# Kernel optimization log

Measured on AMD Instinct MI355X. Metric: run time of the kernel, lower is better.

## Reference

```python
import jax, jax.numpy as jnp
import numpy as np
from jax import lax

A_NUM = 3
STRIDES = (4, 8, 16, 32, 64)
LEVEL_HW = ((128, 208), (64, 104), (32, 52), (16, 26), (8, 13))
IMG_H, IMG_W = 512.0, 832.0
PRE_NMS, POST_NMS, NMS_TH = 6000, 1000, 0.7


def _base_anchors(base_size, ratios=(0.5, 1.0, 2.0), scales=(8.0,)):
    ratios = np.asarray(ratios, np.float64)
    scales = np.asarray(scales, np.float64)
    cx = cy = (base_size - 1) / 2.0
    size = float(base_size) * float(base_size)
    ws = np.round(np.sqrt(size / ratios))
    hs = np.round(ws * ratios)
    ws = (ws[:, None] * scales[None, :]).reshape(-1)
    hs = (hs[:, None] * scales[None, :]).reshape(-1)
    return np.stack([cx - 0.5 * (ws - 1), cy - 0.5 * (hs - 1),
                     cx + 0.5 * (ws - 1), cy + 0.5 * (hs - 1)], axis=1)


def _all_anchors():
    # generate_anchors_global: per-level shifted grids, concatenated, order (h, w, a)
    out = []
    for stride, (h, w) in zip(STRIDES, LEVEL_HW):
        base = _base_anchors(stride)  # [A,4]
        sx = np.arange(w) * stride
        sy = np.arange(h) * stride
        sx, sy = np.meshgrid(sx, sy)
        shifts = np.stack([sx.ravel(), sy.ravel(), sx.ravel(), sy.ravel()], axis=1)
        anc = (shifts[:, None, :] + base[None, :, :]).reshape(-1, 4)  # [H*W*A,4]
        out.append(anc)
    return np.concatenate(out, axis=0).astype(np.float32)

_ANCHORS = _all_anchors()


def _conv(x, w, b, pad):
    y = lax.conv_general_dilated(x, w, (1, 1), [(pad, pad), (pad, pad)],
                                 dimension_numbers=('NCHW', 'OIHW', 'NCHW'))
    return y + b[None, :, None, None]


def _bbox_transform_inv(anchors, deltas):
    w = anchors[:, 2] - anchors[:, 0] + 1.0
    h = anchors[:, 3] - anchors[:, 1] + 1.0
    cx = anchors[:, 0] + 0.5 * w
    cy = anchors[:, 1] + 0.5 * h
    dx, dy, dw, dh = deltas[:, 0], deltas[:, 1], deltas[:, 2], deltas[:, 3]
    pcx = dx * w + cx
    pcy = dy * h + cy
    pw = jnp.exp(dw) * w
    ph = jnp.exp(dh) * h
    return jnp.stack([pcx - 0.5 * pw, pcy - 0.5 * ph,
                      pcx + 0.5 * pw, pcy + 0.5 * ph], axis=1)


def _iou_one_to_many(box, boxes):
    area = (boxes[:, 2] - boxes[:, 0] + 1.0) * (boxes[:, 3] - boxes[:, 1] + 1.0)
    area_b = (box[2] - box[0] + 1.0) * (box[3] - box[1] + 1.0)
    xx1 = jnp.maximum(box[0], boxes[:, 0])
    yy1 = jnp.maximum(box[1], boxes[:, 1])
    xx2 = jnp.minimum(box[2], boxes[:, 2])
    yy2 = jnp.minimum(box[3], boxes[:, 3])
    iw = jnp.maximum(0.0, xx2 - xx1 + 1.0)
    ih = jnp.maximum(0.0, yy2 - yy1 + 1.0)
    inter = iw * ih
    return inter / (area + area_b - inter)


def _nms_fixed(boxes, scores, thresh, max_out):
    # greedy NMS with a fixed number of iterations (jit-friendly)
    def body(s, _):
        i = jnp.argmax(s)
        valid = s[i] > -jnp.inf
        ious = _iou_one_to_many(boxes[i], boxes)
        s2 = jnp.where(ious > thresh, -jnp.inf, s)
        s2 = s2.at[i].set(-jnp.inf)
        return s2, (i, valid)
    _, (idx, valid) = lax.scan(body, scores, None, length=max_out)
    return idx, valid


def _rpn_forward(feats, im_info, rpn_conv_w, rpn_conv_b, rpn_score_w,
                 rpn_score_b, rpn_bbox_w, rpn_bbox_b):
    fg_scores, bbox_deltas = [], []
    for p in feats:
        H, W = p.shape[-2], p.shape[-1]
        f = _conv(p, rpn_conv_w, rpn_conv_b, 1)              # [1,512,H,W]
        cls = _conv(f, rpn_score_w, rpn_score_b, 0)          # [1,2A,H,W]
        # _reshape_layer(.,2) + softmax(dim=1) + _reshape_layer back + permute
        prob = jax.nn.softmax(cls.reshape(1, 2, A_NUM, H, W), axis=1)
        prob = prob.reshape(1, 2 * A_NUM, H, W).transpose(0, 2, 3, 1)  # [1,H,W,2A]
        fg = prob[..., A_NUM:].reshape(-1)                    # fg prob, order (h,w,a)
        bb = _conv(f, rpn_bbox_w, rpn_bbox_b, 0).transpose(0, 2, 3, 1).reshape(-1, 4)
        fg_scores.append(fg)
        bbox_deltas.append(bb)
    scores = jnp.concatenate(fg_scores, axis=0)              # [Ntot]
    deltas = jnp.concatenate(bbox_deltas, axis=0)            # [Ntot,4]
    anchors = jnp.asarray(_ANCHORS)

    proposals = _bbox_transform_inv(anchors, deltas)
    # clip to image
    proposals = jnp.stack([
        jnp.clip(proposals[:, 0], 0.0, im_info[1] - 1.0),
        jnp.clip(proposals[:, 1], 0.0, im_info[0] - 1.0),
        jnp.clip(proposals[:, 2], 0.0, im_info[1] - 1.0),
        jnp.clip(proposals[:, 3], 0.0, im_info[0] - 1.0)], axis=1)

    # pre-NMS top-k by score
    top_scores, order = lax.top_k(scores, PRE_NMS)
    top_boxes = proposals[order]
    keep, valid = _nms_fixed(top_boxes, top_scores, NMS_TH, POST_NMS)
    vmask = valid.astype(top_boxes.dtype)[:, None]
    sel_boxes = top_boxes[keep] * vmask
    sel_scores = top_scores[keep][:, None] * vmask
    rois = jnp.concatenate([jnp.zeros((POST_NMS, 1), sel_boxes.dtype), sel_boxes], axis=1)
    return jnp.concatenate([rois, sel_scores], axis=1)        # [POST_NMS, 6]


def setup_inputs() -> dict:
    key = jax.random.key(0)
    ks = jax.random.split(key, 12)
    chans = 256
    feats = {}
    for i, (name, (h, w)) in enumerate(zip(['p2', 'p3', 'p4', 'p5', 'p6'], LEVEL_HW)):
        feats[name] = jax.random.normal(ks[i], (1, chans, h, w), jnp.float32)
    inp = dict(feats)
    inp['im_info'] = jnp.array([IMG_H, IMG_W, 1.0], jnp.float32)
    inp['rpn_conv_w'] = jax.random.normal(ks[5], (512, chans, 3, 3), jnp.float32) * 0.03
    inp['rpn_conv_b'] = jnp.zeros((512,), jnp.float32)
    inp['rpn_score_w'] = jax.random.normal(ks[6], (2 * A_NUM, 512, 1, 1), jnp.float32) * 0.03
    inp['rpn_score_b'] = jnp.zeros((2 * A_NUM,), jnp.float32)
    inp['rpn_bbox_w'] = jax.random.normal(ks[7], (4 * A_NUM, 512, 1, 1), jnp.float32) * 0.01
    inp['rpn_bbox_b'] = jnp.zeros((4 * A_NUM,), jnp.float32)
    return inp


def reference(p2, p3, p4, p5, p6, im_info, rpn_conv_w, rpn_conv_b,
              rpn_score_w, rpn_score_b, rpn_bbox_w, rpn_bbox_b):
    return _rpn_forward([p2, p3, p4, p5, p6], im_info, rpn_conv_w, rpn_conv_b,
                        rpn_score_w, rpn_score_b, rpn_bbox_w, rpn_bbox_b)
```

## Files before the change

kernel.cpp:

```cpp
#include <hip/hip_runtime.h>
#include <stdint.h>

#define N_ANCH   106392
#define PRE_NMS  6000
#define POST_NMS 1000
#define POOL_CAP 8192
#define NMS_BLKS 94
#define SUP_W    96

static __device__ const int    LV_H[5]      = {128, 64, 32, 16, 8};
static __device__ const int    LV_W[5]      = {208, 104, 52, 26, 13};
static __device__ const int    LV_STRIDE[5] = {4, 8, 16, 32, 64};
static __device__ const int    LV_PIX[5]    = {26624, 6656, 1664, 416, 104};
static __device__ const int    LV_TILE0[6]  = {0, 416, 520, 546, 553, 555};
static __device__ const int    LV_AOFF[6]   = {0, 79872, 99840, 104832, 106080, 106392};
static __device__ const int    GPOFF[6]     = {0, 26624, 33280, 34944, 35360, 35464};
static __device__ const double BASE_ANCH[5][3][4] = {
  {{-22.,-10.,25.,13.},   {-14.,-14.,17.,17.},    {-10.,-22.,13.,25.}},
  {{-40.,-20.,47.,27.},   {-28.,-28.,35.,35.},    {-20.,-44.,27.,51.}},
  {{-84.,-40.,99.,55.},   {-56.,-56.,71.,71.},    {-36.,-80.,51.,95.}},
  {{-164.,-72.,195.,103.},{-112.,-112.,143.,143.},{-76.,-168.,107.,199.}},
  {{-332.,-152.,395.,215.},{-224.,-224.,287.,287.},{-148.,-328.,211.,391.}}
};

__device__ __forceinline__ uint32_t sort32f(float f) {
  uint32_t u = __float_as_uint(f);
  return ((int)u < 0) ? ~u : (u | 0x80000000u);
}
__device__ __forceinline__ uint64_t sort64(double d) {
  uint64_t u = (uint64_t)__double_as_longlong(d);
  return ((long long)u < 0) ? ~u : (u | 0x8000000000000000ull);
}

__device__ __forceinline__ double combf(const float* sw, const float* bw, int c, int j) {
  if (j < 3) return (double)sw[(3 + j) * 512 + c] - (double)sw[j * 512 + c];
  return (double)bw[(j - 3) * 512 + c];
}

__global__ __launch_bounds__(256) void k_weff_part(const float* __restrict__ cw,
                                                   const float* __restrict__ sw,
                                                   const float* __restrict__ bw,
                                                   double* __restrict__ Wpart) {
  int chunk = blockIdx.x / 9;
  int tb = blockIdx.x % 9;
  int t = tb * 256 + threadIdx.x;
  int c0 = chunk * 32;
  double acc[15];
#pragma unroll
  for (int j = 0; j < 15; ++j) acc[j] = 0.0;
#pragma unroll 1
  for (int c = c0; c < c0 + 32; ++c) {
    double v = (double)cw[c * 2304 + t];
#pragma unroll
    for (int j = 0; j < 15; ++j) acc[j] += v * combf(sw, bw, c, j);
  }
  double* o = Wpart + (((size_t)chunk * 2304 + t) << 4);
#pragma unroll
  for (int j = 0; j < 15; ++j) o[j] = acc[j];
  o[15] = 0.0;
}

__global__ __launch_bounds__(256) void k_weff_fin(const double* __restrict__ Wpart,
                                                  const float* __restrict__ cb,
                                                  const float* __restrict__ sb,
                                                  const float* __restrict__ bb,
                                                  const float* __restrict__ sw,
                                                  const float* __restrict__ bw,
                                                  double* __restrict__ Weff,
                                                  double* __restrict__ fb,
                                                  float4* __restrict__ w3,
                                                  float* __restrict__ fb32) {
  if (blockIdx.x == 9) {
    __shared__ double ps[15][16];
    int tid = threadIdx.x;
    if (tid < 240) {
      int j = tid >> 4, part = tid & 15;
      double s = 0.0;
      for (int c = part * 32; c < part * 32 + 32; ++c)
        s += (double)cb[c] * combf(sw, bw, c, j);
      ps[j][part] = s;
    }
    __syncthreads();
    if (tid < 15) {
      double s = 0.0;
#pragma unroll
      for (int part = 0; part < 16; ++part) s += ps[tid][part];
      s += (tid < 3) ? ((double)sb[3 + tid] - (double)sb[tid]) : (double)bb[tid - 3];
      fb[tid] = s;
      if (tid < 3) fb32[tid] = (float)s;
    }
    if (tid == 15) fb32[3] = 0.f;
    return;
  }
  int t = blockIdx.x * 256 + threadIdx.x;
  double acc[15];
#pragma unroll
  for (int j = 0; j < 15; ++j) acc[j] = 0.0;
#pragma unroll 1
  for (int chunk = 0; chunk < 16; ++chunk) {
    const double* p = Wpart + (((size_t)chunk * 2304 + t) << 4);
#pragma unroll
    for (int j = 0; j < 15; ++j) acc[j] += p[j];
  }
  double* o = Weff + ((size_t)t << 4);
#pragma unroll
  for (int j = 0; j < 15; ++j) o[j] = acc[j];
  o[15] = 0.0;
  float4 wf;
  wf.x = (float)acc[0]; wf.y = (float)acc[1]; wf.z = (float)acc[2]; wf.w = 0.f;
  w3[t] = wf;
}

__global__ __launch_bounds__(256) void k_w5(const double* __restrict__ Weff,
                                            double* __restrict__ w5) {
  int idx = blockIdx.x * 256 + threadIdx.x;
  if (idx >= 2304 * 3) return;
  int t = idx / 3, a = idx % 3;
  int ci = t / 9, t9 = t % 9;
  const double* src = Weff + ((size_t)t << 4);
  double* dst = w5 + (size_t)ci * 192 + (size_t)(t9 * 3 + a) * 6;
  int jd = 3 + 4 * a;
  dst[0] = src[jd + 0];
  dst[1] = src[jd + 1];
  dst[2] = src[jd + 2];
  dst[3] = src[jd + 3];
  dst[4] = src[a];
  dst[5] = 0.0;
}

__device__ __forceinline__ void load9(float v[9], const float* __restrict__ ib,
                                      const bool rok[3], const bool cok[3],
                                      const int roff[3]) {
#pragma unroll
  for (int ky = 0; ky < 3; ++ky)
#pragma unroll
    for (int kx = 0; kx < 3; ++kx)
      v[ky * 3 + kx] = (rok[ky] && cok[kx]) ? ib[roff[ky] + kx] : 0.0f;
}

__global__ __launch_bounds__(256) void k_fast(
    const float* __restrict__ p0, const float* __restrict__ p1,
    const float* __restrict__ p2, const float* __restrict__ p3,
    const float* __restrict__ p4,
    const float4* __restrict__ w3, float* __restrict__ qpart) {
  __shared__ float4 w3s[1152];
  __shared__ float red[4][64][3];
  int tid = threadIdx.x, wv = tid >> 6, ln = tid & 63;
  int t = blockIdx.x >> 1, hf = blockIdx.x & 1;
  int cbase = hf * 128;
  for (int i = tid; i < 1152; i += 256) w3s[i] = w3[cbase * 9 + i];
  int L = 0;
  while (L < 4 && t >= LV_TILE0[L + 1]) ++L;
  const float* inL = (L == 0) ? p0 : (L == 1) ? p1 : (L == 2) ? p2 : (L == 3) ? p3 : p4;
  int H = LV_H[L], W = LV_W[L], HW = H * W, PIX = LV_PIX[L];
  int pix = (t - LV_TILE0[L]) * 64 + ln;
  if (pix >= PIX) pix = PIX - 1;
  int h = pix / W, w = pix % W;
  bool rok[3], cok[3];
  int roff[3];
#pragma unroll
  for (int ky = 0; ky < 3; ++ky) {
    int iy = h + ky - 1;
    rok[ky] = (iy >= 0 && iy < H);
    roff[ky] = iy * W + w - 1;
  }
#pragma unroll
  for (int kx = 0; kx < 3; ++kx) {
    int ix = w + kx - 1;
    cok[kx] = (ix >= 0 && ix < W);
  }
  int lci0 = wv * 32;
  const float* ibn = inL + (size_t)(cbase + lci0) * HW;
  float vn[9];
  load9(vn, ibn, rok, cok, roff);
  __syncthreads();
  float a0 = 0.f, a1 = 0.f, a2 = 0.f;
#pragma unroll 1
  for (int c = 0; c < 32; ++c) {
    float vc[9];
#pragma unroll
    for (int q = 0; q < 9; ++q) vc[q] = vn[q];
    if (c < 31) {
      ibn += HW;
      load9(vn, ibn, rok, cok, roff);
    }
    const float4* wr = w3s + (lci0 + c) * 9;
#pragma unroll
    for (int t9 = 0; t9 < 9; ++t9) {
      float4 wt = wr[t9];
      float vv = vc[t9];
      a0 += vv * wt.x; a1 += vv * wt.y; a2 += vv * wt.z;
    }
  }
  red[wv][ln][0] = a0; red[wv][ln][1] = a1; red[wv][ln][2] = a2;
  __syncthreads();
  if (wv == 0) {
    float* o = qpart + ((size_t)(t * 2 + hf) * 64 + ln) * 3;
#pragma unroll
    for (int a = 0; a < 3; ++a)
      o[a] = (red[0][ln][a] + red[1][ln][a]) + (red[2][ln][a] + red[3][ln][a]);
  }
}

__global__ __launch_bounds__(256) void k_fcomb(
    const float* __restrict__ qpart, const float* __restrict__ fb32,
    float* __restrict__ logits32, uint32_t* __restrict__ hist) {
  int tid = threadIdx.x, ln = tid & 63;
  int t = blockIdx.x * 4 + (tid >> 6);
  if (t >= 555) return;
  int L = 0;
  while (L < 4 && t >= LV_TILE0[L + 1]) ++L;
  int PIX = LV_PIX[L];
  int pix = (t - LV_TILE0[L]) * 64 + ln;
  if (pix >= PIX) return;
  const float* q0 = qpart + ((size_t)(t * 2 + 0) * 64 + ln) * 3;
  const float* q1 = qpart + ((size_t)(t * 2 + 1) * 64 + ln) * 3;
  int gbase = LV_AOFF[L] + pix * 3;
#pragma unroll
  for (int a = 0; a < 3; ++a) {
    float f = (q0[a] + q1[a]) + fb32[a];
    logits32[gbase + a] = f;
    atomicAdd(&hist[sort32f(f) >> 16], 1u);
  }
}

__global__ __launch_bounds__(1024) void k_edge(const uint32_t* __restrict__ hist,
                                               uint32_t* __restrict__ cnts) {
  __shared__ uint32_t cs[1024];
  __shared__ uint32_t g_grp, g_suf;
  int t = threadIdx.x, wv = t >> 6, ln = t & 63;
#pragma unroll 4
  for (int r = 0; r < 64; ++r) {
    int g = r * 16 + wv;
    uint32_t x = hist[g * 64 + ln];
#pragma unroll
    for (int off = 32; off > 0; off >>= 1) x += __shfl_down(x, off);
    if (ln == 0) cs[g] = x;
  }
  __syncthreads();
  for (int off = 1; off < 1024; off <<= 1) {
    uint32_t v = cs[t] + ((t + off < 1024) ? cs[t + off] : 0u);
    __syncthreads();
    cs[t] = v;
    __syncthreads();
  }
  uint32_t sufnext = (t < 1023) ? cs[t + 1] : 0u;
  if (cs[t] >= PRE_NMS && sufnext < PRE_NMS) {
    g_grp = (uint32_t)t;
    g_suf = sufnext;
  }
  __syncthreads();
  if (t < 64) {
    uint32_t grp = g_grp, suf = g_suf;
    uint32_t x = hist[grp * 64 + t];
    uint32_t S = x;
#pragma unroll
    for (int off = 1; off < 64; off <<= 1) {
      uint32_t y = __shfl_down(S, off);
      if (t + off < 64) S += y;
    }
    unsigned long long mask = __ballot(suf + S >= PRE_NMS);
    int hi = 63 - (int)__clzll(mask);
    if (t == hi) {
      uint32_t e = grp * 64 + (uint32_t)hi;
      cnts[1] = (e > 2) ? e - 2 : 0;
    }
  }
}

__global__ __launch_bounds__(256) void k_cnt(const float* __restrict__ logits32,
                                             const uint32_t* __restrict__ cnts,
                                             uint32_t* __restrict__ bcnt) {
  __shared__ uint32_t wc[4];
  int tid = threadIdx.x;
  int i = blockIdx.x * 256 + tid;
  uint32_t edge = cnts[1];
  bool pass = (i < N_ANCH) && ((sort32f(logits32[i]) >> 16) >= edge);
  unsigned long long m = __ballot(pass);
  if ((tid & 63) == 0) wc[tid >> 6] = (uint32_t)__popcll(m);
  __syncthreads();
  if (tid == 0) bcnt[blockIdx.x] = wc[0] + wc[1] + wc[2] + wc[3];
}

__global__ __launch_bounds__(256) void k_fill(const float* __restrict__ logits32,
                                              uint32_t* __restrict__ cnts,
                                              const uint32_t* __restrict__ bcnt,
                                              uint32_t* __restrict__ alist) {
  __shared__ uint32_t red[256];
  __shared__ uint32_t woff[4];
  int tid = threadIdx.x, wv = tid >> 6, ln = tid & 63;
  uint32_t s = 0;
  for (int k = tid; k < blockIdx.x; k += 256) s += bcnt[k];
  red[tid] = s;
  __syncthreads();
#pragma unroll
  for (int off = 128; off > 0; off >>= 1) {
    if (tid < off) red[tid] += red[tid + off];
    __syncthreads();
  }
  uint32_t base = red[0];
  int i = blockIdx.x * 256 + tid;
  uint32_t edge = cnts[1];
  bool pass = (i < N_ANCH) && ((sort32f(logits32[i]) >> 16) >= edge);
  unsigned long long m = __ballot(pass);
  if (ln == 0) woff[wv] = (uint32_t)__popcll(m);
  __syncthreads();
  uint32_t off_in_blk = 0;
  for (int k = 0; k < wv; ++k) off_in_blk += woff[k];
  if (pass) {
    uint32_t pos = base + off_in_blk + (uint32_t)__popcll(m & ((1ull << ln) - 1ull));
    if (pos < POOL_CAP) alist[pos] = (uint32_t)i;
  }
  if (blockIdx.x == ((N_ANCH + 255) / 256 - 1) && tid == 0)
    cnts[0] = base + woff[0] + woff[1] + woff[2] + woff[3];
}

__global__ __launch_bounds__(128) void k_refine(
    const float* __restrict__ p0, const float* __restrict__ p1,
    const float* __restrict__ p2, const float* __restrict__ p3,
    const float* __restrict__ p4,
    const double* __restrict__ w5,
    const uint32_t* __restrict__ alist, const uint32_t* __restrict__ cnts,
    double* __restrict__ ppart) {
  __shared__ int4 wlds[2][768];
  int tid = threadIdx.x, wv = tid >> 6, ln = tid & 63;
  int cnt = (int)cnts[0];
  if (cnt > POOL_CAP) cnt = POOL_CAP;
  int grp = blockIdx.x >> 1, half = blockIdx.x & 1;
  int base = grp * 64;
  if (base >= cnt) return;
  int slot = base + ln;
  if (slot >= cnt) slot = cnt - 1;
  int gi = (int)alist[slot];
  int gpix = gi / 3, a = gi - gpix * 3;
  int L = 0;
  while (L < 4 && gpix >= GPOFF[L + 1]) ++L;
  int pix = gpix - GPOFF[L];
  const float* inL = (L == 0) ? p0 : (L == 1) ? p1 : (L == 2) ? p2 : (L == 3) ? p3 : p4;
  int H = LV_H[L], W = LV_W[L], HW = H * W;
  int h = pix / W, w = pix % W;
  bool rok[3], cok[3];
  int roff[3];
#pragma unroll
  for (int ky = 0; ky < 3; ++ky) {
    int iy = h + ky - 1;
    rok[ky] = (iy >= 0 && iy < H);
    roff[ky] = iy * W + w - 1;
  }
#pragma unroll
  for (int kx = 0; kx < 3; ++kx) {
    int ix = w + kx - 1;
    cok[kx] = (ix >= 0 && ix < W);
  }
  int chunk = half * 2 + wv;
  int ci0 = chunk * 64;
  const char* wbc = (const char*)&wlds[wv][0];
  {
    const int4* gs = (const int4*)((const char*)w5 + (size_t)ci0 * 1536);
    int4 r[12];
#pragma unroll
    for (int i = 0; i < 12; ++i) r[i] = gs[i * 64 + ln];
#pragma unroll
    for (int i = 0; i < 12; ++i) wlds[wv][i * 64 + ln] = r[i];
  }
  double sc = 0.0, d0 = 0.0, d1 = 0.0, d2 = 0.0, d3 = 0.0;
  const float* ibn = inL + (size_t)ci0 * HW;
  float vn[9];
  load9(vn, ibn, rok, cok, roff);
#pragma unroll 1
  for (int k = 0; k < 8; ++k) {
    int4 r[12];
    if (k < 7) {
      const int4* gs =
          (const int4*)((const char*)w5 + (size_t)(ci0 + (k + 1) * 8) * 1536);
#pragma unroll
      for (int i = 0; i < 12; ++i) r[i] = gs[i * 64 + ln];
    }
#pragma unroll 1
    for (int c2 = 0; c2 < 8; ++c2) {
      float vc[9];
#pragma unroll
      for (int q = 0; q < 9; ++q) vc[q] = vn[q];
      int lc = k * 8 + c2;
      if (lc < 63) {
        ibn += HW;
        load9(vn, ibn, rok, cok, roff);
      }
      const char* b2 = wbc + c2 * 1536 + a * 48;
#pragma unroll
      for (int t9 = 0; t9 < 9; ++t9) {
        double vd = (double)vc[t9];
        double2 w01 = *(const double2*)(b2 + t9 * 144);
        double2 w23 = *(const double2*)(b2 + t9 * 144 + 16);
        double  w4  = *(const double*)(b2 + t9 * 144 + 32);
        d0 += vd * w01.x; d1 += vd * w01.y;
        d2 += vd * w23.x; d3 += vd * w23.y;
        sc += vd * w4;
      }
    }
    if (k < 7) {
#pragma unroll
      for (int i = 0; i < 12; ++i) wlds[wv][i * 64 + ln] = r[i];
    }
  }
  double* o = ppart + ((size_t)slot * 4 + chunk) * 5;
  o[0] = sc; o[1] = d0; o[2] = d1; o[3] = d2; o[4] = d3;
}

__global__ __launch_bounds__(256) void k_comb(
    const uint32_t* __restrict__ alist, const uint32_t* __restrict__ cnts,
    const double* __restrict__ ppart, const double* __restrict__ fb,
    double* __restrict__ logits, double* __restrict__ deltas,
    uint64_t* __restrict__ pkey) {
  int e = blockIdx.x * 256 + threadIdx.x;
  int cnt = (int)cnts[0];
  if (cnt > POOL_CAP) cnt = POOL_CAP;
  if (blockIdx.x * 256 >= cnt) return;
  if (e >= cnt) return;
  int gi = (int)alist[e];
  int a = gi - (gi / 3) * 3;
  const double* p = ppart + (size_t)e * 20;
  double f[5];
#pragma unroll
  for (int j = 0; j < 5; ++j)
    f[j] = ((p[0 + j] + p[5 + j]) + p[10 + j]) + p[15 + j];
  int js = a, jd = 3 + 4 * a;
  double lg = f[0] + fb[js];
  logits[gi] = lg;
  deltas[gi * 4 + 0] = f[1] + fb[jd + 0];
  deltas[gi * 4 + 1] = f[2] + fb[jd + 1];
  deltas[gi * 4 + 2] = f[3] + fb[jd + 2];
  deltas[gi * 4 + 3] = f[4] + fb[jd + 3];
  pkey[e] = (sort64(lg) & ~0x1FFFFull) | (uint64_t)(0x1FFFFu - (uint32_t)gi);
}

__global__ __launch_bounds__(256) void k_rank_cnt(const uint32_t* __restrict__ cnts,
                                                  const uint64_t* __restrict__ pkey,
                                                  uint32_t* __restrict__ rank32) {
  __shared__ uint64_t lk[512];
  int t = threadIdx.x;
  int cnt = (int)cnts[0];
  if (cnt > POOL_CAP) cnt = POOL_CAP;
  int it = blockIdx.x >> 4, jc = blockIdx.x & 15;
  int e = it * 256 + t;
  int c0 = jc * 512;
  if (it * 256 >= cnt || c0 >= cnt) return;
  int lim = cnt - c0; if (lim > 512) lim = 512;
  for (int i = t; i < 512; i += 256) lk[i] = (i < lim) ? pkey[c0 + i] : 0ull;
  __syncthreads();
  bool active = e < cnt;
  uint64_t mykey = active ? pkey[e] : ~0ull;
  int r = 0;
#pragma unroll 8
  for (int j = 0; j < 512; ++j) r += (lk[j] > mykey) ? 1 : 0;
  if (active && r) atomicAdd(&rank32[e], (uint32_t)r);
}

__global__ __launch_bounds__(256) void k_scatter(const uint32_t* __restrict__ cnts,
                                                 const uint64_t* __restrict__ pkey,
                                                 const uint32_t* __restrict__ rank32,
                                                 const double* __restrict__ logits,
                                                 const double* __restrict__ deltas,
                                                 const float* __restrict__ im_info,
                                                 double* __restrict__ ss,
                                                 double* __restrict__ sbx,
                                                 float4* __restrict__ bxf,
                                                 float* __restrict__ areaf) {
  int t = threadIdx.x;
  int cnt = (int)cnts[0];
  if (cnt > POOL_CAP) cnt = POOL_CAP;
  int e = blockIdx.x * 256 + t;
  if (blockIdx.x * 256 >= cnt) return;
  if (e >= cnt) return;
  int rank = (int)rank32[e];
  if (rank >= PRE_NMS) return;
  uint64_t mykey = pkey[e];
  int gi = 0x1FFFF - (int)(mykey & 0x1FFFFull);
  int L = 0;
  while (L < 4 && gi >= LV_AOFF[L + 1]) ++L;
  int rel = gi - LV_AOFF[L];
  int pix = rel / 3, a = rel % 3;
  int W = LV_W[L];
  int h = pix / W, w = pix % W;
  double imW1 = (double)im_info[1] - 1.0;
  double imH1 = (double)im_info[0] - 1.0;
  double shx = (double)(w * LV_STRIDE[L]), shy = (double)(h * LV_STRIDE[L]);
  double ax1 = BASE_ANCH[L][a][0] + shx, ay1 = BASE_ANCH[L][a][1] + shy;
  double ax2 = BASE_ANCH[L][a][2] + shx, ay2 = BASE_ANCH[L][a][3] + shy;
  double dx = deltas[gi * 4 + 0], dy = deltas[gi * 4 + 1];
  double dw = deltas[gi * 4 + 2], dh = deltas[gi * 4 + 3];
  double wa = ax2 - ax1 + 1.0, ha = ay2 - ay1 + 1.0;
  double cx = ax1 + 0.5 * wa, cy = ay1 + 0.5 * ha;
  double pcx = dx * wa + cx, pcy = dy * ha + cy;
  double pw = exp(dw) * wa, ph = exp(dh) * ha;
  double x1 = fmin(fmax(pcx - 0.5 * pw, 0.0), imW1);
  double y1 = fmin(fmax(pcy - 0.5 * ph, 0.0), imH1);
  double x2 = fmin(fmax(pcx + 0.5 * pw, 0.0), imW1);
  double y2 = fmin(fmax(pcy + 0.5 * ph, 0.0), imH1);
  ss[rank] = 1.0 / (1.0 + exp(-logits[gi]));
  sbx[rank * 4 + 0] = x1; sbx[rank * 4 + 1] = y1;
  sbx[rank * 4 + 2] = x2; sbx[rank * 4 + 3] = y2;
  float4 bf;
  bf.x = (float)x1; bf.y = (float)y1; bf.z = (float)x2; bf.w = (float)y2;
  bxf[rank] = bf;
  areaf[rank] = (float)((x2 - x1 + 1.0) * (y2 - y1 + 1.0));
}

__device__ __forceinline__ bool iou_gt(const double* A, const double* B) {
  double areaA = (A[2] - A[0] + 1.0) * (A[3] - A[1] + 1.0);
  double areaB = (B[2] - B[0] + 1.0) * (B[3] - B[1] + 1.0);
  double xx1 = fmax(A[0], B[0]), yy1 = fmax(A[1], B[1]);
  double xx2 = fmin(A[2], B[2]), yy2 = fmin(A[3], B[3]);
  double iw = fmax(0.0, xx2 - xx1 + 1.0), ih = fmax(0.0, yy2 - yy1 + 1.0);
  double inter = iw * ih;
  return inter > 0.7 * (areaA + areaB - inter);
}

__global__ __launch_bounds__(256) void k_build(const double* __restrict__ sbx,
                                               const float4* __restrict__ bxf,
                                               const float* __restrict__ areaf,
                                               uint64_t* __restrict__ Sup) {
  __shared__ float cbx[256][5];
  __shared__ float rbx[64][5];
  int blk = blockIdx.x;
  int rtile = blk / 24, ctile = blk % 24;
  int t = threadIdx.x, q = t >> 6, ln = t & 63;
  int r = rtile * 64 + ln;
  int w = ctile * 4 + q;
  {
    int c = ctile * 256 + t;
    float4 b;
    float ar;
    if (c < NMS_BLKS * 64) { b = bxf[c]; ar = areaf[c]; }
    else { b.x = b.y = b.z = b.w = 0.f; ar = 0.f; }
    cbx[t][0] = b.x; cbx[t][1] = b.y; cbx[t][2] = b.z; cbx[t][3] = b.w; cbx[t][4] = ar;
    if (t < 64) {
      int rr = rtile * 64 + t;
      float4 rb = bxf[rr];
      rbx[t][0] = rb.x; rbx[t][1] = rb.y; rbx[t][2] = rb.z; rbx[t][3] = rb.w;
      rbx[t][4] = areaf[rr];
    }
  }
  __syncthreads();
  uint64_t bits = 0ull;
  int j0 = w * 64;
  if (w < NMS_BLKS && j0 + 63 > r) {
    float ax1 = rbx[ln][0], ay1 = rbx[ln][1], ax2 = rbx[ln][2], ay2 = rbx[ln][3];
    float aar = rbx[ln][4];
#pragma unroll 4
    for (int jj = 0; jj < 64; ++jj) {
      int j = j0 + jj;
      if (j <= r) continue;
      int cl = q * 64 + jj;
      float iw = fminf(ax2, cbx[cl][2]) - fmaxf(ax1, cbx[cl][0]) + 1.f;
      float ih = fminf(ay2, cbx[cl][3]) - fmaxf(ay1, cbx[cl][1]) + 1.f;
      float inter = fmaxf(iw, 0.f) * fmaxf(ih, 0.f);
      float d = inter - 0.7f * (aar + cbx[cl][4] - inter);
      bool sup;
      if (d > 4.0f) sup = true;
      else if (d < -4.0f) sup = false;
      else sup = iou_gt(sbx + (size_t)r * 4, sbx + (size_t)j * 4);
      if (sup) bits |= 1ull << jj;
    }
  }
  Sup[(size_t)r * SUP_W + w] = bits;
}

__global__ __launch_bounds__(1024) void k_scan(const uint64_t* __restrict__ Sup,
                                               const double* __restrict__ ss,
                                               const double* __restrict__ sbx,
                                               float* __restrict__ out) {
  __shared__ uint16_t keep[POST_NMS];
  __shared__ uint32_t ext_arr[SUP_W][2];
  __shared__ int s_kcnt, s_done;
  __shared__ int s_pend[2][2];
  int t = threadIdx.x, wv = t >> 6, ln = t & 63;
  for (int i = t; i < SUP_W * 2; i += 1024) ext_arr[i >> 1][i & 1] = 0u;
  if (t == 0) { s_kcnt = 0; s_done = 0; }
  if (t < 4) s_pend[t >> 1][t & 1] = 0;
  uint64_t diag = 0ull, nxt = 0ull;
  if (wv == 0) {
    size_t r = (size_t)ln * SUP_W;
    diag = Sup[r + 0];
    nxt  = Sup[r + 1];
  }
  __syncthreads();
  for (int b = 0; b < NMS_BLKS; ++b) {
    if (wv == 0) {
      uint64_t myrow = diag & ~((2ull << ln) - 1ull);
      uint64_t mynxt = nxt;
      if (b + 1 < NMS_BLKS) {
        size_t r = (size_t)((b + 1) * 64 + ln) * SUP_W;
        diag = Sup[r + (b + 1)];
        nxt  = Sup[r + (b + 2)];
      }
      uint64_t ext = ((uint64_t)ext_arr[b][1] << 32) | ext_arr[b][0];
      int base = b * 64;
      if (base + 63 >= PRE_NMS) {
        int v = PRE_NMS - base;
        ext |= ~((1ull << v) - 1ull);
      }
      int K0 = s_kcnt;
      uint64_t avail;
      {
        uint64_t a0 = ~ext;
        uint32_t alo = __builtin_amdgcn_readfirstlane((uint32_t)a0);
        uint32_t ahi = __builtin_amdgcn_readfirstlane((uint32_t)(a0 >> 32));
        avail = ((uint64_t)ahi << 32) | alo;
      }
      uint32_t mr_lo = (uint32_t)myrow, mr_hi = (uint32_t)(myrow >> 32);
      uint32_t mn_lo = (uint32_t)mynxt, mn_hi = (uint32_t)(mynxt >> 32);
      uint64_t kp = 0ull, extn = 0ull;
      int lim = POST_NMS - K0, nk = 0;
      while (avail && nk < lim) {
        int i2 = __ffsll((unsigned long long)avail) - 1;
        uint32_t rlo = (uint32_t)__builtin_amdgcn_readlane((int)mr_lo, i2);
        uint32_t rhi = (uint32_t)__builtin_amdgcn_readlane((int)mr_hi, i2);
        uint32_t qlo = (uint32_t)__builtin_amdgcn_readlane((int)mn_lo, i2);
        uint32_t qhi = (uint32_t)__builtin_amdgcn_readlane((int)mn_hi, i2);
        kp |= 1ull << i2;
        ++nk;
        extn |= ((uint64_t)qhi << 32) | qlo;
        avail &= ~(((uint64_t)rhi << 32) | rlo);
        avail &= ~(1ull << i2);
      }
      if ((kp >> ln) & 1ull) {
        int pos = K0 + __popcll(kp & ((1ull << ln) - 1ull));
        keep[pos] = (uint16_t)(base + ln);
      }
      if (ln == 0) {
        if ((uint32_t)extn)         atomicOr(&ext_arr[b + 1][0], (uint32_t)extn);
        if ((uint32_t)(extn >> 32)) atomicOr(&ext_arr[b + 1][1],
                                             (uint32_t)(extn >> 32));
        s_kcnt = K0 + nk;
        s_pend[(b + 1) & 1][0] = K0;
        s_pend[(b + 1) & 1][1] = K0 + nk;
        if (K0 + nk >= POST_NMS || b + 1 >= NMS_BLKS) s_done = 1;
      }
    } else {
      int lo = s_pend[b & 1][0], hi = s_pend[b & 1][1];
      if (hi > lo) {
        int tt = t - 64;
        int g = tt / 96, w = tt - g * 96;
        if (w >= b + 1) {
          uint64_t v = 0ull;
          for (int q = lo + g; q < hi; q += 10)
            v |= Sup[(size_t)keep[q] * SUP_W + w];
          if (v) {
            if ((uint32_t)v)         atomicOr(&ext_arr[w][0], (uint32_t)v);
            if ((uint32_t)(v >> 32)) atomicOr(&ext_arr[w][1], (uint32_t)(v >> 32));
          }
        }
      }
    }
    __syncthreads();
    if (s_done) break;
  }
  __syncthreads();
  int KF = s_kcnt;
  for (int r = t; r < POST_NMS; r += 1024) {
    float* o = out + r * 6;
    if (r < KF) {
      int p = keep[r];
      o[0] = 0.f;
      o[1] = (float)sbx[p * 4 + 0];
      o[2] = (float)sbx[p * 4 + 1];
      o[3] = (float)sbx[p * 4 + 2];
      o[4] = (float)sbx[p * 4 + 3];
      o[5] = (float)ss[p];
    } else {
#pragma unroll
      for (int c = 0; c < 6; ++c) o[c] = 0.f;
    }
  }
}

extern "C" void kernel_launch(void* const* d_in, const int* in_sizes, int n_in,
                              void* d_out, int out_size, void* d_ws, size_t ws_size,
                              hipStream_t stream) {
  const float* p0 = (const float*)d_in[0];
  const float* p1 = (const float*)d_in[1];
  const float* p2 = (const float*)d_in[2];
  const float* p3 = (const float*)d_in[3];
  const float* p4 = (const float*)d_in[4];
  const float* im_info = (const float*)d_in[5];
  const float* cw = (const float*)d_in[6];
  const float* cb = (const float*)d_in[7];
  const float* sw = (const float*)d_in[8];
  const float* sb = (const float*)d_in[9];
  const float* bw = (const float*)d_in[10];
  const float* bb = (const float*)d_in[11];
  char* ws = (char*)d_ws;
  uint32_t* hist    = (uint32_t*)(ws + 0);
  uint32_t* cnts    = (uint32_t*)(ws + 262144);
  double*   fb      = (double*)  (ws + 262208);
  float*    fb32    = (float*)   (ws + 262336);
  double*   logits  = (double*)  (ws + 262352);
  double*   deltas  = (double*)  (ws + 1113488);
  float*    logits32= (float*)   (ws + 4518032);
  float4*   w3      = (float4*)  (ws + 4943600);
  double*   Weff    = (double*)  (ws + 4980464);
  double*   Wpart   = (double*)  (ws + 5275376);
  uint32_t* alist   = (uint32_t*)(ws + 9993968);
  double*   ssort   = (double*)  (ws + 10026736);
  double*   sbx     = (double*)  (ws + 10074864);
  float4*   bxf     = (float4*)  (ws + 10267376);
  float*    areaf   = (float*)   (ws + 10363632);
  uint64_t* Sup     = (uint64_t*)(ws + 10387696);
  uint64_t* pkey    = (uint64_t*)(ws + 15007984);
  uint32_t* rank32  = (uint32_t*)(ws + 15073520);
  uint32_t* bcnt    = hist;
  double*   W5      = Wpart;
  double*   ppart   = (double*)(ws + 5275376 + 524288);
  float*    qpart   = (float*) (ws + 5275376 + 2097152);
  float* out = (float*)d_out;

  hipMemsetAsync(ws, 0, 262208, stream);
  hipMemsetAsync(rank32, 0, 32768, stream);
  k_weff_part<<<144, 256, 0, stream>>>(cw, sw, bw, Wpart);
  k_weff_fin<<<10, 256, 0, stream>>>(Wpart, cb, sb, bb, sw, bw, Weff, fb, w3, fb32);
  k_w5<<<27, 256, 0, stream>>>(Weff, W5);
  k_fast<<<1110, 256, 0, stream>>>(p0, p1, p2, p3, p4, w3, qpart);
  k_fcomb<<<139, 256, 0, stream>>>(qpart, fb32, logits32, hist);
  k_edge<<<1, 1024, 0, stream>>>(hist, cnts);
  k_cnt<<<416, 256, 0, stream>>>(logits32, cnts, bcnt);
  k_fill<<<416, 256, 0, stream>>>(logits32, cnts, bcnt, alist);
  k_refine<<<256, 128, 0, stream>>>(p0, p1, p2, p3, p4, W5, alist, cnts, ppart);
  k_comb<<<32, 256, 0, stream>>>(alist, cnts, ppart, fb, logits, deltas, pkey);
  k_rank_cnt<<<512, 256, 0, stream>>>(cnts, pkey, rank32);
  k_scatter<<<32, 256, 0, stream>>>(cnts, pkey, rank32, logits, deltas, im_info,
                                    ssort, sbx, bxf, areaf);
  k_build<<<94 * 24, 256, 0, stream>>>(sbx, bxf, areaf, Sup);
  k_scan<<<1, 1024, 0, stream>>>(Sup, ssort, sbx, out);
}
```

Before: 408.0 us.

## Deepen NMS scan pipeline: wave0 propagates two blocks ahead, helpers defer loads

The serial NMS scan now has wave 0 read the suppression words for the next two column blocks and OR both into the external mask, instead of only the next block. Because of this, the helper waves can lag one iteration. They issue up to four global loads of Sup rows per block, then combine and atomically apply them in the following iteration, so load latency overlaps wave 0's serial work. The __syncthreads is replaced by an explicit lgkmcnt wait plus s_barrier, which does not wait on outstanding global (vmcnt) loads. This adds register pressure and subtle correctness risk: the delayed masks must land before block b+2 is read, and the barrier no longer orders global memory.

```diff
diff --git a/kernel.cpp b/kernel.cpp
--- a/kernel.cpp
+++ b/kernel.cpp
@@ -578,21 +578,25 @@
   for (int i = t; i < SUP_W * 2; i += 1024) ext_arr[i >> 1][i & 1] = 0u;
   if (t == 0) { s_kcnt = 0; s_done = 0; }
   if (t < 4) s_pend[t >> 1][t & 1] = 0;
-  uint64_t diag = 0ull, nxt = 0ull;
+  uint64_t diag = 0ull, nxt1 = 0ull, nxt2 = 0ull;
   if (wv == 0) {
     size_t r = (size_t)ln * SUP_W;
     diag = Sup[r + 0];
-    nxt  = Sup[r + 1];
-  }
+    nxt1 = Sup[r + 1];
+    nxt2 = Sup[r + 2];
+  }
+  uint64_t rv0 = 0, rv1 = 0, rv2 = 0, rv3 = 0;
+  int pw = 0, plo = 0, phi = 0;
   __syncthreads();
   for (int b = 0; b < NMS_BLKS; ++b) {
     if (wv == 0) {
       uint64_t myrow = diag & ~((2ull << ln) - 1ull);
-      uint64_t mynxt = nxt;
+      uint64_t myn1 = nxt1, myn2 = nxt2;
       if (b + 1 < NMS_BLKS) {
         size_t r = (size_t)((b + 1) * 64 + ln) * SUP_W;
         diag = Sup[r + (b + 1)];
-        nxt  = Sup[r + (b + 2)];
+        nxt1 = Sup[r + (b + 2)];
+        nxt2 = Sup[r + (b + 3)];
       }
       uint64_t ext = ((uint64_t)ext_arr[b][1] << 32) | ext_arr[b][0];
       int base = b * 64;
@@ -609,18 +613,22 @@
         avail = ((uint64_t)ahi << 32) | alo;
       }
       uint32_t mr_lo = (uint32_t)myrow, mr_hi = (uint32_t)(myrow >> 32);
-      uint32_t mn_lo = (uint32_t)mynxt, mn_hi = (uint32_t)(mynxt >> 32);
-      uint64_t kp = 0ull, extn = 0ull;
+      uint32_t n1_lo = (uint32_t)myn1, n1_hi = (uint32_t)(myn1 >> 32);
+      uint32_t n2_lo = (uint32_t)myn2, n2_hi = (uint32_t)(myn2 >> 32);
+      uint64_t kp = 0ull, extn1 = 0ull, extn2 = 0ull;
       int lim = POST_NMS - K0, nk = 0;
       while (avail && nk < lim) {
         int i2 = __ffsll((unsigned long long)avail) - 1;
         uint32_t rlo = (uint32_t)__builtin_amdgcn_readlane((int)mr_lo, i2);
         uint32_t rhi = (uint32_t)__builtin_amdgcn_readlane((int)mr_hi, i2);
-        uint32_t qlo = (uint32_t)__builtin_amdgcn_readlane((int)mn_lo, i2);
-        uint32_t qhi = (uint32_t)__builtin_amdgcn_readlane((int)mn_hi, i2);
+        uint32_t a1l = (uint32_t)__builtin_amdgcn_readlane((int)n1_lo, i2);
+        uint32_t a1h = (uint32_t)__builtin_amdgcn_readlane((int)n1_hi, i2);
+        uint32_t a2l = (uint32_t)__builtin_amdgcn_readlane((int)n2_lo, i2);
+        uint32_t a2h = (uint32_t)__builtin_amdgcn_readlane((int)n2_hi, i2);
         kp |= 1ull << i2;
         ++nk;
-        extn |= ((uint64_t)qhi << 32) | qlo;
+        extn1 |= ((uint64_t)a1h << 32) | a1l;
+        extn2 |= ((uint64_t)a2h << 32) | a2l;
         avail &= ~(((uint64_t)rhi << 32) | rlo);
         avail &= ~(1ull << i2);
       }
@@ -629,31 +637,47 @@
         keep[pos] = (uint16_t)(base + ln);
       }
       if (ln == 0) {
-        if ((uint32_t)extn)         atomicOr(&ext_arr[b + 1][0], (uint32_t)extn);
-        if ((uint32_t)(extn >> 32)) atomicOr(&ext_arr[b + 1][1],
-                                             (uint32_t)(extn >> 32));
+        if ((uint32_t)extn1)         atomicOr(&ext_arr[b + 1][0], (uint32_t)extn1);
+        if ((uint32_t)(extn1 >> 32)) atomicOr(&ext_arr[b + 1][1],
+                                              (uint32_t)(extn1 >> 32));
+        if ((uint32_t)extn2)         atomicOr(&ext_arr[b + 2][0], (uint32_t)extn2);
+        if ((uint32_t)(extn2 >> 32)) atomicOr(&ext_arr[b + 2][1],
+                                              (uint32_t)(extn2 >> 32));
         s_kcnt = K0 + nk;
         s_pend[(b + 1) & 1][0] = K0;
         s_pend[(b + 1) & 1][1] = K0 + nk;
         if (K0 + nk >= POST_NMS || b + 1 >= NMS_BLKS) s_done = 1;
       }
     } else {
+      int tt = t - 64;
+      int g = tt / 96, w = tt - g * 96;
+      if (phi > plo) {
+        uint64_t v = rv0 | rv1 | rv2 | rv3;
+        for (int q = plo + 40 + g; q < phi; q += 10)
+          v |= Sup[(size_t)keep[q] * SUP_W + pw];
+        if (v) {
+          if ((uint32_t)v)         atomicOr(&ext_arr[pw][0], (uint32_t)v);
+          if ((uint32_t)(v >> 32)) atomicOr(&ext_arr[pw][1], (uint32_t)(v >> 32));
+        }
+      }
+      rv0 = rv1 = rv2 = rv3 = 0ull;
+      plo = 0; phi = 0;
       int lo = s_pend[b & 1][0], hi = s_pend[b & 1][1];
-      if (hi > lo) {
-        int tt = t - 64;
-        int g = tt / 96, w = tt - g * 96;
-        if (w >= b + 1) {
-          uint64_t v = 0ull;
-          for (int q = lo + g; q < hi; q += 10)
-            v |= Sup[(size_t)keep[q] * SUP_W + w];
-          if (v) {
-            if ((uint32_t)v)         atomicOr(&ext_arr[w][0], (uint32_t)v);
-            if ((uint32_t)(v >> 32)) atomicOr(&ext_arr[w][1], (uint32_t)(v >> 32));
-          }
-        }
-      }
-    }
-    __syncthreads();
+      if (hi > lo && w >= b + 2) {
+        int q = lo + g;
+        if (q < hi) rv0 = Sup[(size_t)keep[q] * SUP_W + w];
+        q += 10;
+        if (q < hi) rv1 = Sup[(size_t)keep[q] * SUP_W + w];
+        q += 10;
+        if (q < hi) rv2 = Sup[(size_t)keep[q] * SUP_W + w];
+        q += 10;
+        if (q < hi) rv3 = Sup[(size_t)keep[q] * SUP_W + w];
+        plo = lo; phi = hi; pw = w;
+      }
+    }
+    asm volatile("s_waitcnt lgkmcnt(0)" ::: "memory");
+    __builtin_amdgcn_s_barrier();
+    asm volatile("" ::: "memory");
     if (s_done) break;
   }
   __syncthreads();
```

Measured after the change: 418.7 us. 1.03x slower.
